# Optimization experiments

Hardware: AMD Instinct MI355X
Metric: run time of the kernel (lower is better)

The kernel has to match this reference:

```python
import jax, jax.numpy as jnp
import numpy as np

B = 128
D = 128            # d_model
LENS = [512, 256, 128, 64]   # finest -> coarsest level lengths
ORDERS = [1, 2, 3, 4]        # front_block order, then front_blocks[0..2] orders


def freq_interp(x, target_len):
    # x: (B, C, L_in) -> (B, C, target_len). Zero-pad spectrum, scale by len ratio.
    l_in = x.shape[2]
    xf = jnp.fft.rfft(x, axis=2)                                  # (B,C,l_in//2+1)
    pad = target_len // 2 + 1 - xf.shape[2]
    of = jnp.pad(xf, ((0, 0), (0, 0), (0, pad)))
    out = jnp.fft.irfft(of, n=target_len, axis=2)
    return out * (l_in / target_len)


def cheby_kan(x, coeffs):
    # x: (B,N,C_in), coeffs: (C_in, C_out, deg+1). T_k(t) = cos(k*acos(t)).
    deg1 = coeffs.shape[2]
    theta = jnp.arccos(jnp.tanh(jnp.tanh(x)))                     # (B,N,C_in)
    basis = jnp.cos(theta[..., None] * jnp.arange(deg1, dtype=x.dtype))  # (B,N,C_in,deg+1)
    return jnp.einsum('bnid,iod->bno', basis, coeffs)


def dw_conv(x, w):
    # depthwise Conv1d, kernel 3, padding 1, no bias. x: (B,N,C), w: (C,3).
    xc = jnp.transpose(x, (0, 2, 1))                              # (B,C,N)
    k = w[:, None, :]                                             # (C,1,3) OIH
    y = jax.lax.conv_general_dilated(
        xc, k, window_strides=(1,), padding=[(1, 1)],
        dimension_numbers=('NCH', 'OIH', 'NCH'),
        feature_group_count=x.shape[2])
    return jnp.transpose(y, (0, 2, 1))


def m_kan(x, coeffs, w):
    return cheby_kan(x, coeffs) + dw_conv(x, w)


def setup_inputs():
    key = jax.random.key(0)
    ks = jax.random.split(key, 16)
    inp = {}
    for i, L in enumerate(LENS):
        inp[f'x{i}'] = jax.random.normal(ks[i], (B, L, D), dtype=jnp.float32)
    for j, order in enumerate(ORDERS):
        std = 1.0 / (D * (order + 1))
        inp[f'coeffs{j}'] = std * jax.random.normal(ks[4 + 2 * j], (D, D, order + 1), dtype=jnp.float32)
        inp[f'w{j}'] = 0.1 * jax.random.normal(ks[5 + 2 * j], (D, 3), dtype=jnp.float32)
    return inp


def reference(x0, x1, x2, x3,
              coeffs0, w0, coeffs1, w1, coeffs2, w2, coeffs3, w3):
    levels = [x0, x1, x2, x3]
    rev_lens = LENS[::-1]                      # [64, 128, 256, 512]

    # ---- FrequencyDecomp ----
    rev = levels[::-1]
    out_low, out_high = rev[0], rev[1]
    dec = [out_low]
    for i in range(len(rev) - 1):
        res = jnp.transpose(
            freq_interp(jnp.transpose(out_low, (0, 2, 1)), rev_lens[i + 1]), (0, 2, 1))
        dec.append(out_high - res)
        out_low = out_high
        if i + 2 <= len(rev) - 1:
            out_high = rev[i + 2]
    dec = dec[::-1]

    # ---- FrequencyMixing ----
    rev = dec[::-1]
    out_low = m_kan(rev[0], coeffs0, w0)       # front_block, order=begin_order
    out_high = rev[1]
    blocks = [(coeffs1, w1), (coeffs2, w2), (coeffs3, w3)]
    mix = [out_low]
    for i in range(len(rev) - 1):
        oh = m_kan(out_high, *blocks[i])
        res = jnp.transpose(
            freq_interp(jnp.transpose(out_low, (0, 2, 1)), rev_lens[i + 1]), (0, 2, 1))
        out_low = oh + res
        mix.append(out_low)
        if i + 2 <= len(rev) - 1:
            out_high = rev[i + 2]
    mix = mix[::-1]
    return tuple(mix)
```

## Files before the change

### kernel.cpp

```cpp
#include <hip/hip_runtime.h>
#include <math.h>

#define B_SZ 128
#define D_SZ 128

typedef __attribute__((ext_vector_type(8))) short bf16x8;
typedef __attribute__((ext_vector_type(4))) float f32x4;

__device__ __forceinline__ unsigned short f2bf(float f) {
    unsigned u = __float_as_uint(f);
    unsigned r = (u + 0x7FFF + ((u >> 16) & 1)) >> 16;
    return (unsigned short)r;
}

__device__ __forceinline__ float fast_tanh(float x) {
    float e2 = __builtin_amdgcn_exp2f(x * 2.885390081777927f);
    return fmaf(-2.0f, __builtin_amdgcn_rcpf(e2 + 1.0f), 1.0f);
}

__device__ __forceinline__ void gload_lds16(const unsigned short* g,
                                            unsigned short* l) {
    __builtin_amdgcn_global_load_lds(
        (const __attribute__((address_space(1))) unsigned int*)g,
        (__attribute__((address_space(3))) unsigned int*)l, 16, 0, 0);
}

__device__ __forceinline__ void castT_tile(
    const float* __restrict__ src, unsigned short* __restrict__ dst,
    int b, int n0, int L)
{
    __shared__ unsigned short tt[128][72];
    const int tid = threadIdx.x;
    for (int i = tid; i < 64 * 32; i += 256) {
        int nr = i >> 5, c4 = (i & 31) * 4;
        float4 v = *(const float4*)(src + ((size_t)b * L + n0 + nr) * 128 + c4);
        tt[c4 + 0][nr] = f2bf(v.x);
        tt[c4 + 1][nr] = f2bf(v.y);
        tt[c4 + 2][nr] = f2bf(v.z);
        tt[c4 + 3][nr] = f2bf(v.w);
    }
    __syncthreads();
    const int c = tid >> 1, seg = (tid & 1) * 32;
    unsigned short* dp = dst + ((size_t)b * 128 + c) * L + n0 + seg;
    #pragma unroll
    for (int j = 0; j < 32; j += 8)
        *(bf16x8*)(dp + j) = *(const bf16x8*)&tt[c][seg + j];
}

__global__ __launch_bounds__(256) void prep_all(
    const float* __restrict__ x1, const float* __restrict__ x2,
    const float* __restrict__ x3,
    unsigned short* __restrict__ Xt1, unsigned short* __restrict__ Xt2,
    unsigned short* __restrict__ Xt3,
    unsigned short* __restrict__ U256, unsigned short* __restrict__ U128,
    unsigned short* __restrict__ U64p,
    const float* __restrict__ c0, const float* __restrict__ c1,
    const float* __restrict__ c2, const float* __restrict__ c3,
    unsigned short* __restrict__ BmT_all, float* __restrict__ bias_all)
{
    const int bid = blockIdx.x, tid = threadIdx.x;
    if (bid < 896) {
        if (bid < 512)      castT_tile(x1, Xt1, bid >> 2, (bid & 3) * 64, 256);
        else if (bid < 768) castT_tile(x2, Xt2, (bid - 512) >> 1, ((bid - 512) & 1) * 64, 128);
        else                castT_tile(x3, Xt3, bid - 768, 0, 64);
    } else if (bid < 1568) {
        int fid = (bid - 896) * 256 + tid;
        unsigned short* U; int L, lg, e;
        if (fid < 131072)      { U = U256; L = 256; lg = 8; e = fid; }
        else if (fid < 163840) { U = U128; L = 128; lg = 7; e = fid - 131072; }
        else                   { U = U64p; L = 64;  lg = 6; e = fid - 163840; }
        const int n = e & (L - 1);
        const int m = e >> lg;
        const int t = m >> 1;
        const float inv4L = 1.0f / (4.0f * (float)L);
        float val;
        if ((m & 1) == 0) {
            val = ((t == n) ? 0.25f : 0.0f) + (((t + n) & 1) ? -inv4L : inv4L);
        } else {
            int idx = (t - n) & (L - 1);
            double th = M_PI * (2.0 * idx + 1.0) / (2.0 * L);
            double ct = cos(th) / sin(th);
            val = (float)((idx & 1) ? -ct : ct) * inv4L;
        }
        U[e] = f2bf(val);
    } else {
        const int r   = bid - 1568;
        const int set = r >> 6;
        const int o   = ((r & 63) << 1) + (tid >> 7);
        const int i   = tid & 127;
        const int DEG1 = set + 2;
        const float* cc = (set == 0) ? c0 : (set == 1) ? c1 : (set == 2) ? c2 : c3;
        const float* cp = cc + ((size_t)i * 128 + o) * DEG1;
        unsigned short* Bm = BmT_all + (size_t)set * 65536;
        for (int d = 1; d < DEG1; ++d)
            Bm[(size_t)(d - 1) * 16384 + o * 128 + i] = f2bf(cp[d]);
        float s = cp[0];
        #pragma unroll
        for (int off = 32; off >= 1; off >>= 1) s += __shfl_down(s, off);
        __shared__ float red[4];
        if ((tid & 63) == 0) red[tid >> 6] = s;
        __syncthreads();
        if ((tid & 127) == 0)
            bias_all[set * 128 + o] = red[tid >> 6] + red[(tid >> 6) + 1];
    }
}

__device__ __forceinline__ void up2_body(
    const unsigned short* __restrict__ U,
    const unsigned short* __restrict__ Xt,
    const float* __restrict__ xh,
    float* __restrict__ out,
    unsigned short* __restrict__ xtm,
    float sign, int b, int mt, int L)
{
    const int NK = L >> 5;
    const int tid = threadIdx.x;
    __shared__ unsigned short Ab[2][2048];
    __shared__ unsigned short Bb[2][4096];

    const int ln = tid & 63, wv = tid >> 6;
    const int wm = wv & 1, wn = wv >> 1;
    const int lr = ln & 15, qd = ln >> 4;

    f32x4 acc[2][4];
    #pragma unroll
    for (int mi = 0; mi < 2; ++mi)
        #pragma unroll
        for (int nt = 0; nt < 4; ++nt)
            acc[mi][nt] = (f32x4){0.f, 0.f, 0.f, 0.f};

    const int arow = tid >> 2, acol = (tid & 3) * 8;

    auto stage = [&](int kk, int buf) {
        const unsigned short* ga = U + (size_t)(mt * 64 + arow) * L + kk * 32 + acol;
        gload_lds16(ga, (unsigned short*)Ab[buf] + (tid << 3));
        #pragma unroll
        for (int j = 0; j < 2; ++j) {
            int sidx = tid + (j << 8);
            const unsigned short* gb =
                Xt + ((size_t)b * 128 + (sidx >> 2)) * L + kk * 32 + (sidx & 3) * 8;
            gload_lds16(gb, (unsigned short*)Bb[buf] + (sidx << 3));
        }
    };

    stage(0, 0);
    for (int kk = 0; kk < NK; ++kk) {
        __syncthreads();
        if (kk + 1 < NK) stage(kk + 1, (kk + 1) & 1);
        const int buf = kk & 1;
        bf16x8 af[2], bfv[4];
        #pragma unroll
        for (int mi = 0; mi < 2; ++mi)
            af[mi] = *(const bf16x8*)&Ab[buf][(wm * 32 + mi * 16 + lr) * 32 + qd * 8];
        #pragma unroll
        for (int nt = 0; nt < 4; ++nt)
            bfv[nt] = *(const bf16x8*)&Bb[buf][(wn * 64 + nt * 16 + lr) * 32 + qd * 8];
        #pragma unroll
        for (int mi = 0; mi < 2; ++mi)
            #pragma unroll
            for (int nt = 0; nt < 4; ++nt)
                acc[mi][nt] = __builtin_amdgcn_mfma_f32_16x16x32_bf16(
                    af[mi], bfv[nt], acc[mi][nt], 0, 0, 0);
    }

    const int twoL = L << 1;
    #pragma unroll
    for (int nt = 0; nt < 4; ++nt) {
        const int col = wn * 64 + nt * 16 + lr;
        #pragma unroll
        for (int mi = 0; mi < 2; ++mi) {
            #pragma unroll
            for (int r = 0; r < 4; ++r) {
                const int row = mt * 64 + wm * 32 + mi * 16 + qd * 4 + r;
                const size_t gi = ((size_t)b * twoL + row) * 128 + col;
                float v = xh[gi] + sign * acc[mi][nt][r];
                out[gi] = v;
                if (xtm)
                    xtm[((size_t)b * 128 + col) * twoL + row] = f2bf(v);
            }
        }
    }
}

__global__ __launch_bounds__(256) void up2_dec(
    const unsigned short* __restrict__ U64p, const unsigned short* __restrict__ U128,
    const unsigned short* __restrict__ U256,
    const unsigned short* __restrict__ Xt3, const unsigned short* __restrict__ Xt2,
    const unsigned short* __restrict__ Xt1,
    const float* __restrict__ x2, const float* __restrict__ x1,
    const float* __restrict__ x0,
    float* __restrict__ d2, float* __restrict__ d1, float* __restrict__ d0)
{
    const int bid = blockIdx.x;
    const unsigned short *U, *Xt; const float* xh; float* out;
    int L, lgMT, base;
    if (bid < 256)      { U = U64p; Xt = Xt3; xh = x2; out = d2; L = 64;  lgMT = 1; base = 0; }
    else if (bid < 768) { U = U128; Xt = Xt2; xh = x1; out = d1; L = 128; lgMT = 2; base = 256; }
    else                { U = U256; Xt = Xt1; xh = x0; out = d0; L = 256; lgMT = 3; base = 768; }
    const int rb = bid - base;
    up2_body(U, Xt, xh, out, nullptr, -1.f, rb >> lgMT, rb & ((1 << lgMT) - 1), L);
}

__global__ __launch_bounds__(256) void up2_mix(
    const unsigned short* __restrict__ U, const unsigned short* __restrict__ Xt,
    float* __restrict__ m, unsigned short* __restrict__ xtm, int L, int lgMT)
{
    up2_body(U, Xt, m, m, xtm, 1.f,
             blockIdx.x >> lgMT, blockIdx.x & ((1 << lgMT) - 1), L);
}

__global__ __launch_bounds__(256) void mkan_all(
    const float* __restrict__ xa, const float* __restrict__ xb,
    const float* __restrict__ xc, const float* __restrict__ xd,
    const unsigned short* __restrict__ BmT_all,
    const float* __restrict__ bias_all,
    const float* __restrict__ w0p, const float* __restrict__ w1p,
    const float* __restrict__ w2p, const float* __restrict__ w3p,
    float* __restrict__ m0, float* __restrict__ m1,
    float* __restrict__ m2, float* __restrict__ m3,
    unsigned short* __restrict__ xtm0)
{
    __shared__ unsigned short As[16384];
    __shared__ unsigned short Bb[2][4096];

    const int bid = blockIdx.x, tid = threadIdx.x;
    const float *x, *w; float* outp; unsigned short* xtm = nullptr;
    int set, mb, Lmask;
    if (bid < 256)       { x = xa; w = w0p; outp = m0; set = 0; mb = bid << 5;          Lmask = 63;  xtm = xtm0; }
    else if (bid < 768)  { x = xb; w = w1p; outp = m1; set = 1; mb = (bid - 256) << 5;  Lmask = 127; }
    else if (bid < 1792) { x = xc; w = w2p; outp = m2; set = 2; mb = (bid - 768) << 5;  Lmask = 255; }
    else                 { x = xd; w = w3p; outp = m3; set = 3; mb = (bid - 1792) << 5; Lmask = 511; }
    const int deg1m1 = set + 1;
    const int NK = deg1m1 << 2;
    const unsigned short* Bm = BmT_all + (size_t)set * 65536;
    const float* bias = bias_all + (set << 7);

    for (int e = tid * 4; e < 4096; e += 1024) {
        const int row = e >> 7, i = e & 127;
        float4 v = *(const float4*)(x + ((size_t)(mb + row)) * 128 + i);
        float u0 = fast_tanh(fast_tanh(v.x)), u1 = fast_tanh(fast_tanh(v.y));
        float u2 = fast_tanh(fast_tanh(v.z)), u3 = fast_tanh(fast_tanh(v.w));
        float tp0 = 1.f, tp1 = 1.f, tp2 = 1.f, tp3 = 1.f;
        float tc0 = u0, tc1 = u1, tc2 = u2, tc3 = u3;
        unsigned short* ap0 = &As[((i >> 5) << 10) + (row << 5) + (i & 31)];
        for (int p = 0; p < deg1m1; ++p) {
            unsigned short* ap = ap0 + (p << 12);
            ap[0] = f2bf(tc0); ap[1] = f2bf(tc1);
            ap[2] = f2bf(tc2); ap[3] = f2bf(tc3);
            float tn0 = fmaf(2.f * u0, tc0, -tp0); tp0 = tc0; tc0 = tn0;
            float tn1 = fmaf(2.f * u1, tc1, -tp1); tp1 = tc1; tc1 = tn1;
            float tn2 = fmaf(2.f * u2, tc2, -tp2); tp2 = tc2; tc2 = tn2;
            float tn3 = fmaf(2.f * u3, tc3, -tp3); tp3 = tc3; tc3 = tn3;
        }
    }

    const int ln = tid & 63, wv = tid >> 6;
    const int wm = wv & 1, wn = wv >> 1;
    const int lr = ln & 15, qd = ln >> 4;

    f32x4 acc[4];
    #pragma unroll
    for (int nt = 0; nt < 4; ++nt) acc[nt] = (f32x4){0.f, 0.f, 0.f, 0.f};

    auto stageB = [&](int kk, int buf) {
        const int p = kk >> 2, i0 = (kk & 3) << 5;
        #pragma unroll
        for (int j = 0; j < 2; ++j) {
            int sidx = tid + (j << 8);
            const unsigned short* gb =
                Bm + (size_t)((p << 7) + (sidx >> 2)) * 128 + i0 + ((sidx & 3) << 3);
            gload_lds16(gb, (unsigned short*)Bb[buf] + (sidx << 3));
        }
    };

    stageB(0, 0);
    for (int kk = 0; kk < NK; ++kk) {
        __syncthreads();
        if (kk + 1 < NK) stageB(kk + 1, (kk + 1) & 1);
        const int buf = kk & 1;
        bf16x8 af = *(const bf16x8*)&As[(kk << 10) + (((wm << 4) + lr) << 5) + (qd << 3)];
        bf16x8 bfv[4];
        #pragma unroll
        for (int nt = 0; nt < 4; ++nt)
            bfv[nt] = *(const bf16x8*)&Bb[buf][(((wn << 6) + (nt << 4) + lr) << 5) + (qd << 3)];
        #pragma unroll
        for (int nt = 0; nt < 4; ++nt)
            acc[nt] = __builtin_amdgcn_mfma_f32_16x16x32_bf16(af, bfv[nt], acc[nt], 0, 0, 0);
    }

    #pragma unroll
    for (int nt = 0; nt < 4; ++nt) {
        const int col = (wn << 6) + (nt << 4) + lr;
        const float ww0 = w[col * 3 + 0], ww1 = w[col * 3 + 1], ww2 = w[col * 3 + 2];
        const float bs = bias[col];
        #pragma unroll
        for (int r = 0; r < 4; ++r) {
            const int row = (wm << 4) + (qd << 2) + r;
            const int gm = mb + row;
            const int n = gm & Lmask;
            const size_t gi = (size_t)gm * 128 + col;
            float xm1 = (n > 0)     ? x[gi - 128] : 0.f;
            float x0v = x[gi];
            float xp1 = (n < Lmask) ? x[gi + 128] : 0.f;
            float v = acc[nt][r] + bs + fmaf(ww0, xm1, fmaf(ww1, x0v, ww2 * xp1));
            outp[gi] = v;
            if (xtm)
                xtm[(size_t)(((gm >> 6) << 7) + col) * 64 + (gm & 63)] = f2bf(v);
        }
    }
}

extern "C" void kernel_launch(void* const* d_in, const int* in_sizes, int n_in,
                              void* d_out, int out_size, void* d_ws, size_t ws_size,
                              hipStream_t stream) {
    const float* x0 = (const float*)d_in[0];
    const float* x1 = (const float*)d_in[1];
    const float* x2 = (const float*)d_in[2];
    const float* x3 = (const float*)d_in[3];
    const float* c0 = (const float*)d_in[4];
    const float* w0 = (const float*)d_in[5];
    const float* c1 = (const float*)d_in[6];
    const float* w1 = (const float*)d_in[7];
    const float* c2 = (const float*)d_in[8];
    const float* w2 = (const float*)d_in[9];
    const float* c3 = (const float*)d_in[10];
    const float* w3 = (const float*)d_in[11];
    float* out = (float*)d_out;

    float* d0 = (float*)d_ws;
    float* d1 = d0 + 8388608;
    float* d2 = d1 + 4194304;
    unsigned short* Xt1  = (unsigned short*)(d2 + 2097152);
    unsigned short* Xt2  = Xt1 + 4194304;
    unsigned short* Xt3  = Xt2 + 2097152;
    unsigned short* Xtm0 = Xt3 + 1048576;
    unsigned short* Xtm1 = Xtm0 + 1048576;
    unsigned short* Xtm2 = Xtm1 + 2097152;
    unsigned short* BmT  = Xtm2 + 4194304;
    float* bias_all = (float*)(BmT + 262144);
    unsigned short* U256 = (unsigned short*)(bias_all + 512);
    unsigned short* U128 = U256 + 131072;
    unsigned short* U64p = U128 + 32768;

    float* m3 = out;
    float* m2 = m3 + 8388608;
    float* m1 = m2 + 4194304;
    float* m0 = m1 + 2097152;

    prep_all<<<1824, 256, 0, stream>>>(x1, x2, x3, Xt1, Xt2, Xt3,
                                       U256, U128, U64p,
                                       c0, c1, c2, c3, BmT, bias_all);

    up2_dec<<<1792, 256, 0, stream>>>(U64p, U128, U256, Xt3, Xt2, Xt1,
                                      x2, x1, x0, d2, d1, d0);

    mkan_all<<<3840, 256, 0, stream>>>(x3, d2, d1, d0, BmT, bias_all,
                                       w0, w1, w2, w3, m0, m1, m2, m3, Xtm0);

    up2_mix<<<256,  256, 0, stream>>>(U64p, Xtm0, m1, Xtm1, 64, 1);
    up2_mix<<<512,  256, 0, stream>>>(U128, Xtm1, m2, Xtm2, 128, 2);
    up2_mix<<<1024, 256, 0, stream>>>(U256, Xtm2, m3, nullptr, 256, 3);
}
```

Measured before the change: 276.1 us.

## Unroll mixing recurrence into composed upsample operators and compute Chebyshev basis in registers

The sequential mixing chain is replaced by precomposed upsampling matrices (U256·U128·U64 and similar), built by two small compose kernels. mkan_all writes every level's KAN output into one concatenated bf16 buffer, so a single fused launch computes m1, m2 and m3 together, removing two dependent launches and their serialization. The mkan kernel also stores tanh-tanh values in LDS as fp32 and generates the Chebyshev basis in registers inside the MFMA loop, replacing the large bf16 basis tile. In exchange it does larger K GEMMs for the finest level and adds extra bf16 rounding from the composed matrices.

```diff
diff --git a/kernel.cpp b/kernel.cpp
--- a/kernel.cpp
+++ b/kernel.cpp
@@ -1,8 +1,5 @@
 #include <hip/hip_runtime.h>
 #include <math.h>
-
-#define B_SZ 128
-#define D_SZ 128
 
 typedef __attribute__((ext_vector_type(8))) short bf16x8;
 typedef __attribute__((ext_vector_type(4))) float f32x4;
@@ -11,6 +8,10 @@
     unsigned u = __float_as_uint(f);
     unsigned r = (u + 0x7FFF + ((u >> 16) & 1)) >> 16;
     return (unsigned short)r;
+}
+
+__device__ __forceinline__ float bf2f(unsigned short s) {
+    return __uint_as_float(((unsigned)s) << 16);
 }
 
 __device__ __forceinline__ float fast_tanh(float x) {
@@ -105,15 +106,51 @@
     }
 }
 
+__global__ __launch_bounds__(256) void compose1(
+    const unsigned short* __restrict__ U64p, const unsigned short* __restrict__ U128,
+    const unsigned short* __restrict__ U256,
+    unsigned short* __restrict__ Wcat2, unsigned short* __restrict__ Wcat3)
+{
+    int t = blockIdx.x * 256 + threadIdx.x;
+    if (t < 32768) {
+        int m = t >> 7, c = t & 127;
+        Wcat2[m * 192 + c] = U128[t];
+    } else if (t < 49152) {
+        int e = t - 32768, m = e >> 6, q = e & 63;
+        float s = 0.f;
+        for (int n = 0; n < 128; ++n)
+            s += bf2f(U128[m * 128 + n]) * bf2f(U64p[n * 64 + q]);
+        Wcat2[m * 192 + 128 + q] = f2bf(s);
+    } else if (t < 180224) {
+        int e = t - 49152, m = e >> 8, c = e & 255;
+        Wcat3[m * 448 + c] = U256[e];
+    } else if (t < 245760) {
+        int e = t - 180224, m = e >> 7, q = e & 127;
+        float s = 0.f;
+        for (int n = 0; n < 256; ++n)
+            s += bf2f(U256[m * 256 + n]) * bf2f(U128[n * 128 + q]);
+        Wcat3[m * 448 + 256 + q] = f2bf(s);
+    }
+}
+
+__global__ __launch_bounds__(256) void compose2(
+    const unsigned short* __restrict__ U64p, unsigned short* __restrict__ Wcat3)
+{
+    int t = blockIdx.x * 256 + threadIdx.x;
+    int m = t >> 6, q = t & 63;
+    float s = 0.f;
+    for (int n = 0; n < 128; ++n)
+        s += bf2f(Wcat3[m * 448 + 256 + n]) * bf2f(U64p[n * 64 + q]);
+    Wcat3[m * 448 + 384 + q] = f2bf(s);
+}
+
 __device__ __forceinline__ void up2_body(
-    const unsigned short* __restrict__ U,
-    const unsigned short* __restrict__ Xt,
-    const float* __restrict__ xh,
-    float* __restrict__ out,
-    unsigned short* __restrict__ xtm,
-    float sign, int b, int mt, int L)
-{
-    const int NK = L >> 5;
+    const unsigned short* __restrict__ A, int Ars,
+    const unsigned short* __restrict__ Bbase, int Brs, int bOff,
+    const float* __restrict__ xh, float* __restrict__ out,
+    float sign, int b, int mt, int K, int Mrows)
+{
+    const int NK = K >> 5;
     const int tid = threadIdx.x;
     __shared__ unsigned short Ab[2][2048];
     __shared__ unsigned short Bb[2][4096];
@@ -132,13 +169,13 @@
     const int arow = tid >> 2, acol = (tid & 3) * 8;
 
     auto stage = [&](int kk, int buf) {
-        const unsigned short* ga = U + (size_t)(mt * 64 + arow) * L + kk * 32 + acol;
+        const unsigned short* ga = A + (size_t)(mt * 64 + arow) * Ars + kk * 32 + acol;
         gload_lds16(ga, (unsigned short*)Ab[buf] + (tid << 3));
         #pragma unroll
         for (int j = 0; j < 2; ++j) {
             int sidx = tid + (j << 8);
             const unsigned short* gb =
-                Xt + ((size_t)b * 128 + (sidx >> 2)) * L + kk * 32 + (sidx & 3) * 8;
+                Bbase + ((size_t)b * 128 + (sidx >> 2)) * Brs + bOff + kk * 32 + (sidx & 3) * 8;
             gload_lds16(gb, (unsigned short*)Bb[buf] + (sidx << 3));
         }
     };
@@ -163,7 +200,6 @@
                     af[mi], bfv[nt], acc[mi][nt], 0, 0, 0);
     }
 
-    const int twoL = L << 1;
     #pragma unroll
     for (int nt = 0; nt < 4; ++nt) {
         const int col = wn * 64 + nt * 16 + lr;
@@ -172,11 +208,8 @@
             #pragma unroll
             for (int r = 0; r < 4; ++r) {
                 const int row = mt * 64 + wm * 32 + mi * 16 + qd * 4 + r;
-                const size_t gi = ((size_t)b * twoL + row) * 128 + col;
-                float v = xh[gi] + sign * acc[mi][nt][r];
-                out[gi] = v;
-                if (xtm)
-                    xtm[((size_t)b * 128 + col) * twoL + row] = f2bf(v);
+                const size_t gi = ((size_t)b * Mrows + row) * 128 + col;
+                out[gi] = xh[gi] + sign * acc[mi][nt][r];
             }
         }
     }
@@ -198,15 +231,23 @@
     else if (bid < 768) { U = U128; Xt = Xt2; xh = x1; out = d1; L = 128; lgMT = 2; base = 256; }
     else                { U = U256; Xt = Xt1; xh = x0; out = d0; L = 256; lgMT = 3; base = 768; }
     const int rb = bid - base;
-    up2_body(U, Xt, xh, out, nullptr, -1.f, rb >> lgMT, rb & ((1 << lgMT) - 1), L);
-}
-
-__global__ __launch_bounds__(256) void up2_mix(
-    const unsigned short* __restrict__ U, const unsigned short* __restrict__ Xt,
-    float* __restrict__ m, unsigned short* __restrict__ xtm, int L, int lgMT)
-{
-    up2_body(U, Xt, m, m, xtm, 1.f,
-             blockIdx.x >> lgMT, blockIdx.x & ((1 << lgMT) - 1), L);
+    up2_body(U, L, Xt, L, 0, xh, out, -1.f,
+             rb >> lgMT, rb & ((1 << lgMT) - 1), L, L << 1);
+}
+
+__global__ __launch_bounds__(256) void mix_fused(
+    const unsigned short* __restrict__ U64p,
+    const unsigned short* __restrict__ Wcat2, const unsigned short* __restrict__ Wcat3,
+    const unsigned short* __restrict__ Ktall,
+    float* __restrict__ m1, float* __restrict__ m2, float* __restrict__ m3)
+{
+    const int bid = blockIdx.x;
+    const unsigned short* A; float* mo;
+    int Ars, bOff, K, Mrows, b, mt;
+    if (bid < 256)      { A = U64p;  Ars = 64;  bOff = 384; K = 64;  Mrows = 128; mo = m1; b = bid >> 1;          mt = bid & 1; }
+    else if (bid < 768) { A = Wcat2; Ars = 192; bOff = 256; K = 192; Mrows = 256; mo = m2; b = (bid - 256) >> 2;  mt = (bid - 256) & 3; }
+    else                { A = Wcat3; Ars = 448; bOff = 0;   K = 448; Mrows = 512; mo = m3; b = (bid - 768) >> 3;  mt = (bid - 768) & 7; }
+    up2_body(A, Ars, Ktall, 448, bOff, mo, mo, 1.f, b, mt, K, Mrows);
 }
 
 __global__ __launch_bounds__(256) void mkan_all(
@@ -218,52 +259,25 @@
     const float* __restrict__ w2p, const float* __restrict__ w3p,
     float* __restrict__ m0, float* __restrict__ m1,
     float* __restrict__ m2, float* __restrict__ m3,
-    unsigned short* __restrict__ xtm0)
-{
-    __shared__ unsigned short As[16384];
+    unsigned short* __restrict__ Ktall)
+{
+    __shared__ float Us[32][132];
     __shared__ unsigned short Bb[2][4096];
 
     const int bid = blockIdx.x, tid = threadIdx.x;
-    const float *x, *w; float* outp; unsigned short* xtm = nullptr;
-    int set, mb, Lmask;
-    if (bid < 256)       { x = xa; w = w0p; outp = m0; set = 0; mb = bid << 5;          Lmask = 63;  xtm = xtm0; }
-    else if (bid < 768)  { x = xb; w = w1p; outp = m1; set = 1; mb = (bid - 256) << 5;  Lmask = 127; }
-    else if (bid < 1792) { x = xc; w = w2p; outp = m2; set = 2; mb = (bid - 768) << 5;  Lmask = 255; }
+    const float *x, *w; float* outp; unsigned short* kt = nullptr;
+    int set, mb, Lmask, lgL = 9;
+    if (bid < 256)       { x = xa; w = w0p; outp = m0; set = 0; mb = bid << 5;          Lmask = 63;  lgL = 6; kt = Ktall + 384; }
+    else if (bid < 768)  { x = xb; w = w1p; outp = m1; set = 1; mb = (bid - 256) << 5;  Lmask = 127; lgL = 7; kt = Ktall + 256; }
+    else if (bid < 1792) { x = xc; w = w2p; outp = m2; set = 2; mb = (bid - 768) << 5;  Lmask = 255; lgL = 8; kt = Ktall; }
     else                 { x = xd; w = w3p; outp = m3; set = 3; mb = (bid - 1792) << 5; Lmask = 511; }
     const int deg1m1 = set + 1;
     const int NK = deg1m1 << 2;
     const unsigned short* Bm = BmT_all + (size_t)set * 65536;
     const float* bias = bias_all + (set << 7);
 
-    for (int e = tid * 4; e < 4096; e += 1024) {
-        const int row = e >> 7, i = e & 127;
-        float4 v = *(const float4*)(x + ((size_t)(mb + row)) * 128 + i);
-        float u0 = fast_tanh(fast_tanh(v.x)), u1 = fast_tanh(fast_tanh(v.y));
-        float u2 = fast_tanh(fast_tanh(v.z)), u3 = fast_tanh(fast_tanh(v.w));
-        float tp0 = 1.f, tp1 = 1.f, tp2 = 1.f, tp3 = 1.f;
-        float tc0 = u0, tc1 = u1, tc2 = u2, tc3 = u3;
-        unsigned short* ap0 = &As[((i >> 5) << 10) + (row << 5) + (i & 31)];
-        for (int p = 0; p < deg1m1; ++p) {
-            unsigned short* ap = ap0 + (p << 12);
-            ap[0] = f2bf(tc0); ap[1] = f2bf(tc1);
-            ap[2] = f2bf(tc2); ap[3] = f2bf(tc3);
-            float tn0 = fmaf(2.f * u0, tc0, -tp0); tp0 = tc0; tc0 = tn0;
-            float tn1 = fmaf(2.f * u1, tc1, -tp1); tp1 = tc1; tc1 = tn1;
-            float tn2 = fmaf(2.f * u2, tc2, -tp2); tp2 = tc2; tc2 = tn2;
-            float tn3 = fmaf(2.f * u3, tc3, -tp3); tp3 = tc3; tc3 = tn3;
-        }
-    }
-
-    const int ln = tid & 63, wv = tid >> 6;
-    const int wm = wv & 1, wn = wv >> 1;
-    const int lr = ln & 15, qd = ln >> 4;
-
-    f32x4 acc[4];
-    #pragma unroll
-    for (int nt = 0; nt < 4; ++nt) acc[nt] = (f32x4){0.f, 0.f, 0.f, 0.f};
-
-    auto stageB = [&](int kk, int buf) {
-        const int p = kk >> 2, i0 = (kk & 3) << 5;
+    auto stageB = [&](int p, int c4, int buf) {
+        const int i0 = c4 << 5;
         #pragma unroll
         for (int j = 0; j < 2; ++j) {
             int sidx = tid + (j << 8);
@@ -273,19 +287,70 @@
         }
     };
 
-    stageB(0, 0);
-    for (int kk = 0; kk < NK; ++kk) {
-        __syncthreads();
-        if (kk + 1 < NK) stageB(kk + 1, (kk + 1) & 1);
-        const int buf = kk & 1;
-        bf16x8 af = *(const bf16x8*)&As[(kk << 10) + (((wm << 4) + lr) << 5) + (qd << 3)];
-        bf16x8 bfv[4];
-        #pragma unroll
-        for (int nt = 0; nt < 4; ++nt)
-            bfv[nt] = *(const bf16x8*)&Bb[buf][(((wn << 6) + (nt << 4) + lr) << 5) + (qd << 3)];
-        #pragma unroll
-        for (int nt = 0; nt < 4; ++nt)
-            acc[nt] = __builtin_amdgcn_mfma_f32_16x16x32_bf16(af, bfv[nt], acc[nt], 0, 0, 0);
+    stageB(0, 0, 0);
+
+    for (int e = tid * 4; e < 4096; e += 1024) {
+        const int row = e >> 7, i = e & 127;
+        float4 v = *(const float4*)(x + ((size_t)(mb + row)) * 128 + i);
+        float4 r;
+        r.x = fast_tanh(fast_tanh(v.x));
+        r.y = fast_tanh(fast_tanh(v.y));
+        r.z = fast_tanh(fast_tanh(v.z));
+        r.w = fast_tanh(fast_tanh(v.w));
+        *(float4*)&Us[row][i] = r;
+    }
+
+    const int ln = tid & 63, wv = tid >> 6;
+    const int wm = wv & 1, wn = wv >> 1;
+    const int lr = ln & 15, qd = ln >> 4;
+    const int arow = (wm << 4) + lr;
+
+    f32x4 acc[4];
+    #pragma unroll
+    for (int nt = 0; nt < 4; ++nt) acc[nt] = (f32x4){0.f, 0.f, 0.f, 0.f};
+
+    __syncthreads();
+
+    int s = 0;
+    for (int c4 = 0; c4 < 4; ++c4) {
+        const float4 ua = *(const float4*)&Us[arow][(c4 << 5) + (qd << 3)];
+        const float4 ub = *(const float4*)&Us[arow][(c4 << 5) + (qd << 3) + 4];
+        const float u0 = ua.x, u1 = ua.y, u2 = ua.z, u3 = ua.w;
+        const float u4 = ub.x, u5 = ub.y, u6 = ub.z, u7 = ub.w;
+        float tp0 = 1.f, tp1 = 1.f, tp2 = 1.f, tp3 = 1.f;
+        float tp4 = 1.f, tp5 = 1.f, tp6 = 1.f, tp7 = 1.f;
+        float tc0 = u0, tc1 = u1, tc2 = u2, tc3 = u3;
+        float tc4 = u4, tc5 = u5, tc6 = u6, tc7 = u7;
+        for (int p = 0; p < deg1m1; ++p, ++s) {
+            if (s) __syncthreads();
+            if (s + 1 < NK) {
+                int np = p + 1, nc4 = c4;
+                if (np == deg1m1) { np = 0; ++nc4; }
+                stageB(np, nc4, (s + 1) & 1);
+            }
+            union { unsigned int w[4]; bf16x8 v; } afu;
+            asm("v_cvt_pk_bf16_f32 %0, %1, %2" : "=v"(afu.w[0]) : "v"(tc0), "v"(tc1));
+            asm("v_cvt_pk_bf16_f32 %0, %1, %2" : "=v"(afu.w[1]) : "v"(tc2), "v"(tc3));
+            asm("v_cvt_pk_bf16_f32 %0, %1, %2" : "=v"(afu.w[2]) : "v"(tc4), "v"(tc5));
+            asm("v_cvt_pk_bf16_f32 %0, %1, %2" : "=v"(afu.w[3]) : "v"(tc6), "v"(tc7));
+            const int buf = s & 1;
+            bf16x8 bfv[4];
+            #pragma unroll
+            for (int nt = 0; nt < 4; ++nt)
+                bfv[nt] = *(const bf16x8*)&Bb[buf][(((wn << 6) + (nt << 4) + lr) << 5) + (qd << 3)];
+            #pragma unroll
+            for (int nt = 0; nt < 4; ++nt)
+                acc[nt] = __builtin_amdgcn_mfma_f32_16x16x32_bf16(afu.v, bfv[nt], acc[nt], 0, 0, 0);
+            float tn;
+            tn = fmaf(2.f * u0, tc0, -tp0); tp0 = tc0; tc0 = tn;
+            tn = fmaf(2.f * u1, tc1, -tp1); tp1 = tc1; tc1 = tn;
+            tn = fmaf(2.f * u2, tc2, -tp2); tp2 = tc2; tc2 = tn;
+            tn = fmaf(2.f * u3, tc3, -tp3); tp3 = tc3; tc3 = tn;
+            tn = fmaf(2.f * u4, tc4, -tp4); tp4 = tc4; tc4 = tn;
+            tn = fmaf(2.f * u5, tc5, -tp5); tp5 = tc5; tc5 = tn;
+            tn = fmaf(2.f * u6, tc6, -tp6); tp6 = tc6; tc6 = tn;
+            tn = fmaf(2.f * u7, tc7, -tp7); tp7 = tc7; tc7 = tn;
+        }
     }
 
     #pragma unroll
@@ -304,8 +369,8 @@
             float xp1 = (n < Lmask) ? x[gi + 128] : 0.f;
             float v = acc[nt][r] + bs + fmaf(ww0, xm1, fmaf(ww1, x0v, ww2 * xp1));
             outp[gi] = v;
-            if (xtm)
-                xtm[(size_t)(((gm >> 6) << 7) + col) * 64 + (gm & 63)] = f2bf(v);
+            if (kt)
+                kt[(size_t)((gm >> lgL) * 128 + col) * 448 + n] = f2bf(v);
         }
     }
 }
@@ -330,13 +395,13 @@
     float* d0 = (float*)d_ws;
     float* d1 = d0 + 8388608;
     float* d2 = d1 + 4194304;
-    unsigned short* Xt1  = (unsigned short*)(d2 + 2097152);
-    unsigned short* Xt2  = Xt1 + 4194304;
-    unsigned short* Xt3  = Xt2 + 2097152;
-    unsigned short* Xtm0 = Xt3 + 1048576;
-    unsigned short* Xtm1 = Xtm0 + 1048576;
-    unsigned short* Xtm2 = Xtm1 + 2097152;
-    unsigned short* BmT  = Xtm2 + 4194304;
+    unsigned short* Xt1   = (unsigned short*)(d2 + 2097152);
+    unsigned short* Xt2   = Xt1 + 4194304;
+    unsigned short* Xt3   = Xt2 + 2097152;
+    unsigned short* Wcat2 = Xt3;
+    unsigned short* Wcat3 = Wcat2 + 49152;
+    unsigned short* Ktall = Xt3 + 1048576;
+    unsigned short* BmT   = Ktall + 7340032;
     float* bias_all = (float*)(BmT + 262144);
     unsigned short* U256 = (unsigned short*)(bias_all + 512);
     unsigned short* U128 = U256 + 131072;
@@ -354,10 +419,11 @@
     up2_dec<<<1792, 256, 0, stream>>>(U64p, U128, U256, Xt3, Xt2, Xt1,
                                       x2, x1, x0, d2, d1, d0);
 
+    compose1<<<960, 256, 0, stream>>>(U64p, U128, U256, Wcat2, Wcat3);
+    compose2<<<128, 256, 0, stream>>>(U64p, Wcat3);
+
     mkan_all<<<3840, 256, 0, stream>>>(x3, d2, d1, d0, BmT, bias_all,
-                                       w0, w1, w2, w3, m0, m1, m2, m3, Xtm0);
-
-    up2_mix<<<256,  256, 0, stream>>>(U64p, Xtm0, m1, Xtm1, 64, 1);
-    up2_mix<<<512,  256, 0, stream>>>(U128, Xtm1, m2, Xtm2, 128, 2);
-    up2_mix<<<1024, 256, 0, stream>>>(U256, Xtm2, m3, nullptr, 256, 3);
-}
+                                       w0, w1, w2, w3, m0, m1, m2, m3, Ktall);
+
+    mix_fused<<<1792, 256, 0, stream>>>(U64p, Wcat2, Wcat3, Ktall, m1, m2, m3);
+}
```

New measurement: 315.9 us. +14.4%, slower.

## Generate Chebyshev basis fragments in registers inside the MFMA loop

Applied to the files above, without the earlier changes.

Instead of materialising the full bf16 Chebyshev basis matrix in LDS before the GEMM, the kernel stores only the double-tanh values in a padded fp32 LDS tile. Each wave builds its A-fragment directly in registers via the recurrence, converting with packed bf16 instructions. The K loop is reordered to iterate column chunk outer and degree inner, and the first B stage is issued before the tanh prologue. This cuts LDS footprint and A-matrix LDS traffic, and it may raise occupancy. In exchange, each wave recomputes the recurrence for its rows, and it relies on inline asm for the bf16 conversion.

```diff
diff --git a/kernel.cpp b/kernel.cpp
--- a/kernel.cpp
+++ b/kernel.cpp
@@ -1,8 +1,5 @@
 #include <hip/hip_runtime.h>
 #include <math.h>
-
-#define B_SZ 128
-#define D_SZ 128
 
 typedef __attribute__((ext_vector_type(8))) short bf16x8;
 typedef __attribute__((ext_vector_type(4))) float f32x4;
@@ -220,7 +217,7 @@
     float* __restrict__ m2, float* __restrict__ m3,
     unsigned short* __restrict__ xtm0)
 {
-    __shared__ unsigned short As[16384];
+    __shared__ float Us[32][132];
     __shared__ unsigned short Bb[2][4096];
 
     const int bid = blockIdx.x, tid = threadIdx.x;
@@ -235,35 +232,8 @@
     const unsigned short* Bm = BmT_all + (size_t)set * 65536;
     const float* bias = bias_all + (set << 7);
 
-    for (int e = tid * 4; e < 4096; e += 1024) {
-        const int row = e >> 7, i = e & 127;
-        float4 v = *(const float4*)(x + ((size_t)(mb + row)) * 128 + i);
-        float u0 = fast_tanh(fast_tanh(v.x)), u1 = fast_tanh(fast_tanh(v.y));
-        float u2 = fast_tanh(fast_tanh(v.z)), u3 = fast_tanh(fast_tanh(v.w));
-        float tp0 = 1.f, tp1 = 1.f, tp2 = 1.f, tp3 = 1.f;
-        float tc0 = u0, tc1 = u1, tc2 = u2, tc3 = u3;
-        unsigned short* ap0 = &As[((i >> 5) << 10) + (row << 5) + (i & 31)];
-        for (int p = 0; p < deg1m1; ++p) {
-            unsigned short* ap = ap0 + (p << 12);
-            ap[0] = f2bf(tc0); ap[1] = f2bf(tc1);
-            ap[2] = f2bf(tc2); ap[3] = f2bf(tc3);
-            float tn0 = fmaf(2.f * u0, tc0, -tp0); tp0 = tc0; tc0 = tn0;
-            float tn1 = fmaf(2.f * u1, tc1, -tp1); tp1 = tc1; tc1 = tn1;
-            float tn2 = fmaf(2.f * u2, tc2, -tp2); tp2 = tc2; tc2 = tn2;
-            float tn3 = fmaf(2.f * u3, tc3, -tp3); tp3 = tc3; tc3 = tn3;
-        }
-    }
-
-    const int ln = tid & 63, wv = tid >> 6;
-    const int wm = wv & 1, wn = wv >> 1;
-    const int lr = ln & 15, qd = ln >> 4;
-
-    f32x4 acc[4];
-    #pragma unroll
-    for (int nt = 0; nt < 4; ++nt) acc[nt] = (f32x4){0.f, 0.f, 0.f, 0.f};
-
-    auto stageB = [&](int kk, int buf) {
-        const int p = kk >> 2, i0 = (kk & 3) << 5;
+    auto stageB = [&](int p, int c4, int buf) {
+        const int i0 = c4 << 5;
         #pragma unroll
         for (int j = 0; j < 2; ++j) {
             int sidx = tid + (j << 8);
@@ -273,19 +243,70 @@
         }
     };
 
-    stageB(0, 0);
-    for (int kk = 0; kk < NK; ++kk) {
-        __syncthreads();
-        if (kk + 1 < NK) stageB(kk + 1, (kk + 1) & 1);
-        const int buf = kk & 1;
-        bf16x8 af = *(const bf16x8*)&As[(kk << 10) + (((wm << 4) + lr) << 5) + (qd << 3)];
-        bf16x8 bfv[4];
-        #pragma unroll
-        for (int nt = 0; nt < 4; ++nt)
-            bfv[nt] = *(const bf16x8*)&Bb[buf][(((wn << 6) + (nt << 4) + lr) << 5) + (qd << 3)];
-        #pragma unroll
-        for (int nt = 0; nt < 4; ++nt)
-            acc[nt] = __builtin_amdgcn_mfma_f32_16x16x32_bf16(af, bfv[nt], acc[nt], 0, 0, 0);
+    stageB(0, 0, 0);
+
+    for (int e = tid * 4; e < 4096; e += 1024) {
+        const int row = e >> 7, i = e & 127;
+        float4 v = *(const float4*)(x + ((size_t)(mb + row)) * 128 + i);
+        float4 r;
+        r.x = fast_tanh(fast_tanh(v.x));
+        r.y = fast_tanh(fast_tanh(v.y));
+        r.z = fast_tanh(fast_tanh(v.z));
+        r.w = fast_tanh(fast_tanh(v.w));
+        *(float4*)&Us[row][i] = r;
+    }
+
+    const int ln = tid & 63, wv = tid >> 6;
+    const int wm = wv & 1, wn = wv >> 1;
+    const int lr = ln & 15, qd = ln >> 4;
+    const int arow = (wm << 4) + lr;
+
+    f32x4 acc[4];
+    #pragma unroll
+    for (int nt = 0; nt < 4; ++nt) acc[nt] = (f32x4){0.f, 0.f, 0.f, 0.f};
+
+    __syncthreads();
+
+    int s = 0;
+    for (int c4 = 0; c4 < 4; ++c4) {
+        const float4 ua = *(const float4*)&Us[arow][(c4 << 5) + (qd << 3)];
+        const float4 ub = *(const float4*)&Us[arow][(c4 << 5) + (qd << 3) + 4];
+        const float u0 = ua.x, u1 = ua.y, u2 = ua.z, u3 = ua.w;
+        const float u4 = ub.x, u5 = ub.y, u6 = ub.z, u7 = ub.w;
+        float tp0 = 1.f, tp1 = 1.f, tp2 = 1.f, tp3 = 1.f;
+        float tp4 = 1.f, tp5 = 1.f, tp6 = 1.f, tp7 = 1.f;
+        float tc0 = u0, tc1 = u1, tc2 = u2, tc3 = u3;
+        float tc4 = u4, tc5 = u5, tc6 = u6, tc7 = u7;
+        for (int p = 0; p < deg1m1; ++p, ++s) {
+            if (s) __syncthreads();
+            if (s + 1 < NK) {
+                int np = p + 1, nc4 = c4;
+                if (np == deg1m1) { np = 0; ++nc4; }
+                stageB(np, nc4, (s + 1) & 1);
+            }
+            union { unsigned int w[4]; bf16x8 v; } afu;
+            asm("v_cvt_pk_bf16_f32 %0, %1, %2" : "=v"(afu.w[0]) : "v"(tc0), "v"(tc1));
+            asm("v_cvt_pk_bf16_f32 %0, %1, %2" : "=v"(afu.w[1]) : "v"(tc2), "v"(tc3));
+            asm("v_cvt_pk_bf16_f32 %0, %1, %2" : "=v"(afu.w[2]) : "v"(tc4), "v"(tc5));
+            asm("v_cvt_pk_bf16_f32 %0, %1, %2" : "=v"(afu.w[3]) : "v"(tc6), "v"(tc7));
+            const int buf = s & 1;
+            bf16x8 bfv[4];
+            #pragma unroll
+            for (int nt = 0; nt < 4; ++nt)
+                bfv[nt] = *(const bf16x8*)&Bb[buf][(((wn << 6) + (nt << 4) + lr) << 5) + (qd << 3)];
+            #pragma unroll
+            for (int nt = 0; nt < 4; ++nt)
+                acc[nt] = __builtin_amdgcn_mfma_f32_16x16x32_bf16(afu.v, bfv[nt], acc[nt], 0, 0, 0);
+            float tn;
+            tn = fmaf(2.f * u0, tc0, -tp0); tp0 = tc0; tc0 = tn;
+            tn = fmaf(2.f * u1, tc1, -tp1); tp1 = tc1; tc1 = tn;
+            tn = fmaf(2.f * u2, tc2, -tp2); tp2 = tc2; tc2 = tn;
+            tn = fmaf(2.f * u3, tc3, -tp3); tp3 = tc3; tc3 = tn;
+            tn = fmaf(2.f * u4, tc4, -tp4); tp4 = tc4; tc4 = tn;
+            tn = fmaf(2.f * u5, tc5, -tp5); tp5 = tc5; tc5 = tn;
+            tn = fmaf(2.f * u6, tc6, -tp6); tp6 = tc6; tc6 = tn;
+            tn = fmaf(2.f * u7, tc7, -tp7); tp7 = tc7; tc7 = tn;
+        }
     }
 
     #pragma unroll
```

Result: faster. 264.5 us (-4.2%).
